# Kernel optimization log

Hardware: AMD Instinct MI355X
Metric: run time of the kernel (lower is better)

Reference implementation:

```python
import jax, jax.numpy as jnp
import numpy as np

B = 2
NCLS = 19    # semantic classes for the logits heads
NLAB = 20    # raw point label values 0..19 (0 = unlabeled)
# (Z, Y, X) grids at strides 2, 4, 8 of sizes=[256,256,32]
GRIDS = {2: (16, 128, 128), 4: (8, 64, 64), 8: (4, 32, 32)}


def _lin_idx(coord, Z, Y, X):
    # coord: (N,4) int rows [b, z, y, x] -> flat cell index over B*Z*Y*X
    b, z, y, x = coord[:, 0], coord[:, 1], coord[:, 2], coord[:, 3]
    return ((b * Z + z) * Y + y) * X + x


def _bev_projection(feat, coord, Y, X):
    # Fused equivalent of torch.unique + scatter_max + spconv dense():
    # scatter_max features directly into the dense (B, Y, X) BEV grid keyed by (b,y,x).
    key = (coord[:, 0] * Y + coord[:, 2]) * X + coord[:, 3]
    C = feat.shape[1]
    dense = jax.ops.segment_max(feat, key, num_segments=B * Y * X)  # empty cells -> -inf
    dense = jnp.where(jnp.isfinite(dense), dense, jnp.zeros((), feat.dtype))
    return dense.reshape(B, Y, X, C).transpose(0, 3, 1, 2)  # (B, C, Y, X)


def _voxel_sem_target(fcoord, pcoord, plabel, Z, Y, X):
    # Majority-vote semantic label per point voxel, gathered at feature voxel coords.
    ncell = B * Z * Y * X
    pair = _lin_idx(pcoord, Z, Y, X) * NLAB + plabel  # (cell, label) key
    counts = jax.ops.segment_sum(
        jnp.ones(pcoord.shape[0], jnp.int32), pair, num_segments=ncell * NLAB
    ).reshape(ncell, NLAB)
    maj = jnp.argmax(counts, axis=1).astype(jnp.int32)   # most frequent label per cell
    occ = counts.sum(axis=1) > 0                          # cell contains any point
    fk = _lin_idx(fcoord, Z, Y, X)
    return jnp.where(occ[fk], maj[fk], 0).astype(jnp.int32)  # unmatched -> 0


def _head(x, w1, g, b, w2, b2):
    # Linear(no bias) -> BatchNorm1d(train stats) -> LeakyReLU(0.1) -> Linear
    h = x @ w1
    mu = h.mean(axis=0)
    var = h.var(axis=0)
    h = (h - mu) * jax.lax.rsqrt(var + 1e-5) * g + b
    h = jnp.where(h >= 0, h, 0.1 * h)
    return h @ w2 + b2


def _rand_coords(key, n, Z, Y, X):
    kb, kz, ky, kx = jax.random.split(key, 4)
    return jnp.stack([
        jax.random.randint(kb, (n,), 0, B, dtype=jnp.int32),
        jax.random.randint(kz, (n,), 0, Z, dtype=jnp.int32),
        jax.random.randint(ky, (n,), 0, Y, dtype=jnp.int32),
        jax.random.randint(kx, (n,), 0, X, dtype=jnp.int32),
    ], axis=1)


def setup_inputs() -> dict:
    key = jax.random.key(0)
    ks = jax.random.split(key, 32)
    M1, M2, M3, NP = 200000, 100000, 50000, 500000
    inp = {
        'proj1_vw': jax.random.normal(ks[0], (M1, 64), jnp.float32),
        'proj2_vw': jax.random.normal(ks[1], (M2, 128), jnp.float32),
        'proj3_vw': jax.random.normal(ks[2], (M3, 256), jnp.float32),
        'vw1_coord': _rand_coords(ks[3], M1, *GRIDS[2]),
        'vw2_coord': _rand_coords(ks[4], M2, *GRIDS[4]),
        'vw3_coord': _rand_coords(ks[5], M3, *GRIDS[8]),
        'idx02': _rand_coords(ks[6], NP, *GRIDS[2]),
        'idx04': _rand_coords(ks[7], NP, *GRIDS[4]),
        'idx08': _rand_coords(ks[8], NP, *GRIDS[8]),
        'pw_label': jax.random.randint(ks[9], (NP,), 0, NLAB, dtype=jnp.int32),
    }
    # learned head parameters (out2 / out4 / out8)
    def head_params(k, cin):
        k1, k2 = jax.random.split(k)
        return (jax.random.normal(k1, (cin, 64), jnp.float32) * 0.02,
                jnp.ones((64,), jnp.float32), jnp.zeros((64,), jnp.float32),
                jax.random.normal(k2, (64, NCLS), jnp.float32) * 0.02,
                jnp.zeros((NCLS,), jnp.float32))
    for tag, k, cin in (('h2', ks[10], 64), ('h4', ks[11], 128), ('h8', ks[12], 256)):
        w1, g, b, w2, b2 = head_params(k, cin)
        inp[f'{tag}_w1'], inp[f'{tag}_g'], inp[f'{tag}_b'] = w1, g, b
        inp[f'{tag}_w2'], inp[f'{tag}_b2'] = w2, b2
    return inp


def reference(proj1_vw, proj2_vw, proj3_vw, vw1_coord, vw2_coord, vw3_coord,
              idx02, idx04, idx08, pw_label,
              h2_w1, h2_g, h2_b, h2_w2, h2_b2,
              h4_w1, h4_g, h4_b, h4_w2, h4_b2,
              h8_w1, h8_g, h8_b, h8_w2, h8_b2):
    (Z2, Y2, X2), (Z4, Y4, X4), (Z8, Y8, X8) = GRIDS[2], GRIDS[4], GRIDS[8]
    bev1 = _bev_projection(proj1_vw, vw1_coord, Y2, X2)   # (B, 64, 128, 128)
    bev2 = _bev_projection(proj2_vw, vw2_coord, Y4, X4)   # (B, 128, 64, 64)
    bev3 = _bev_projection(proj3_vw, vw3_coord, Y8, X8)   # (B, 256, 32, 32)
    lbl2 = _voxel_sem_target(vw1_coord, idx02, pw_label, Z2, Y2, X2)
    lbl4 = _voxel_sem_target(vw2_coord, idx04, pw_label, Z4, Y4, X4)
    lbl8 = _voxel_sem_target(vw3_coord, idx08, pw_label, Z8, Y8, X8)
    log2 = _head(proj1_vw, h2_w1, h2_g, h2_b, h2_w2, h2_b2)
    log4 = _head(proj2_vw, h4_w1, h4_g, h4_b, h4_w2, h4_b2)
    log8 = _head(proj3_vw, h8_w1, h8_g, h8_b, h8_w2, h8_b2)
    return (bev1, bev2, bev3, log2, log4, log8, lbl2, lbl4, lbl8)
```

## Files before the change

### kernel.cpp

```cpp
#include <hip/hip_runtime.h>
#include <hip/hip_bf16.h>

typedef unsigned int u32;
typedef unsigned short u16;
typedef __attribute__((ext_vector_type(8))) short short8;
typedef __attribute__((ext_vector_type(4))) float f32x4;

#define NLAB 20

#define M_1 200000
#define C_1 64
#define Z_1 16
#define Y_1 128
#define X_1 128

#define M_2 100000
#define C_2 128
#define Z_2 8
#define Y_2 64
#define X_2 64

#define M_3 50000
#define C_3 256
#define Z_3 4
#define Y_3 32
#define X_3 32

#define O_BEV1 0
#define O_BEV2 2097152
#define O_BEV3 3145728
#define O_LOG1 3670016
#define O_LOG2 7470016
#define O_LOG3 9370016
#define O_LBL1 10320016
#define O_LBL2 10520016
#define O_LBL3 10620016

#define WB_CNT 0
#define WB_CUR 43008
#define WB_PIDX 86016
#define NCELLS 43008
#define SB1 0
#define SB2 32768
#define SB3 40960

#define WBEV_F  4194304
#define WBEV2_F 6291456
#define WBEV3_F 7340032

#define WC1_W 8388608
#define WC2_W 11010048
#define WC3_W 11337728
#define W_COUNT_BYTES 11960320ull
#define WH1 0
#define WH2 12800000
#define WH3 19200000
#define WPART 12000000
#define WP1 0
#define WP2 200064
#define WP3 300160
#define WSTATS 12350208

#define GB1 1563
#define GB2 782
#define GB3 391
#define HB1 782
#define HB2 391
#define HB3 196

static __device__ __forceinline__ u16 f2bf(float f) {
  u32 u = __float_as_uint(f);
  u32 r = u + 0x7fffu + ((u >> 16) & 1u);
  return (u16)(r >> 16);
}

__global__ __launch_bounds__(256) void k_cellcount(
    const int* __restrict__ co1, const int* __restrict__ co2, const int* __restrict__ co3,
    int* __restrict__ cnt)
{
  int blk = blockIdx.x;
  const int* co; int Y, X, M, base, m;
  if (blk < HB1)            { co = co1; Y = Y_1; X = X_1; M = M_1; base = SB1; m = blk * 256 + threadIdx.x; }
  else if (blk < HB1 + HB2) { co = co2; Y = Y_2; X = X_2; M = M_2; base = SB2; m = (blk - HB1) * 256 + threadIdx.x; }
  else                      { co = co3; Y = Y_3; X = X_3; M = M_3; base = SB3; m = (blk - HB1 - HB2) * 256 + threadIdx.x; }
  if (m >= M) return;
  int4 c = *(const int4*)(co + m * 4);
  atomicAdd(cnt + base + (c.x * Y + c.z) * X + c.w, 1);
}

__global__ __launch_bounds__(1024) void k_scan(const int* __restrict__ cnt, int* __restrict__ cur) {
  int t = threadIdx.x;
  int local[42];
  int s = 0;
#pragma unroll
  for (int j = 0; j < 42; j++) { local[j] = cnt[t * 42 + j]; s += local[j]; }
  __shared__ int red[1024];
  red[t] = s;
  __syncthreads();
  for (int off = 1; off < 1024; off <<= 1) {
    int v = (t >= off) ? red[t - off] : 0;
    __syncthreads();
    red[t] += v;
    __syncthreads();
  }
  int base = red[t] - s;
#pragma unroll
  for (int j = 0; j < 42; j++) { cur[t * 42 + j] = base; base += local[j]; }
}

__global__ __launch_bounds__(256) void k_scatter(
    const int* __restrict__ co1, const int* __restrict__ co2, const int* __restrict__ co3,
    int* __restrict__ cur, int* __restrict__ pidx)
{
  int blk = blockIdx.x;
  const int* co; int Y, X, M, base, m;
  if (blk < HB1)            { co = co1; Y = Y_1; X = X_1; M = M_1; base = SB1; m = blk * 256 + threadIdx.x; }
  else if (blk < HB1 + HB2) { co = co2; Y = Y_2; X = X_2; M = M_2; base = SB2; m = (blk - HB1) * 256 + threadIdx.x; }
  else                      { co = co3; Y = Y_3; X = X_3; M = M_3; base = SB3; m = (blk - HB1 - HB2) * 256 + threadIdx.x; }
  if (m >= M) return;
  int4 c = *(const int4*)(co + m * 4);
  int slot = atomicAdd(cur + base + (c.x * Y + c.z) * X + c.w, 1);
  pidx[slot] = m;
}

#define GBATCH 8
__global__ __launch_bounds__(256) void k_gc(
    const float* __restrict__ f1, const float* __restrict__ f2, const float* __restrict__ f3,
    const int* __restrict__ cnt, const int* __restrict__ cur,
    const int* __restrict__ pidx, float* __restrict__ ws,
    const int* __restrict__ i2, const int* __restrict__ i4, const int* __restrict__ i8,
    const int* __restrict__ lab, u32* __restrict__ hist)
{
  int blk = blockIdx.x;
  if (blk < 14336) {
    int wid = blk * 4 + (threadIdx.x >> 6);
    int lane = threadIdx.x & 63;
    const float* f; int cidx; size_t wbase; int C;
    if (wid < 32768) {
      f = f1; C = 64; cidx = SB1 + wid; wbase = WBEV_F + (size_t)wid * 64;
    } else if (wid < 49152) {
      int u = wid - 32768; int cell = u >> 1, ch = (u & 1) * 64;
      f = f2 + ch; C = 128; cidx = SB2 + cell; wbase = WBEV2_F + (size_t)cell * 128 + ch;
    } else {
      int u = wid - 49152; int cell = u >> 2, ch = (u & 3) * 64;
      f = f3 + ch; C = 256; cidx = SB3 + cell; wbase = WBEV3_F + (size_t)cell * 256 + ch;
    }
    int n = cnt[cidx], end = cur[cidx];
    float acc = __uint_as_float(0xff800000u);
    for (int i = end - n; i < end; i += GBATCH) {
      int p[GBATCH];
#pragma unroll
      for (int j = 0; j < GBATCH; j++) {
        int idx = i + j;
        p[j] = pidx[idx < end ? idx : end - 1];
      }
      float v[GBATCH];
#pragma unroll
      for (int j = 0; j < GBATCH; j++) v[j] = f[(size_t)p[j] * C + lane];
#pragma unroll
      for (int j = 0; j < GBATCH; j++) acc = fmaxf(acc, v[j]);
    }
    ws[wbase + lane] = (n > 0) ? acc : 0.f;
  } else {
    int cb = blk - 14336;
    const int* pc; int Z, Y, X; u32* base; int i;
    if (cb < 1954)      { pc = i2; Z = Z_1; Y = Y_1; X = X_1; base = hist + WC1_W; i = cb * 256 + threadIdx.x; }
    else if (cb < 3908) { pc = i4; Z = Z_2; Y = Y_2; X = X_2; base = hist + WC2_W; i = (cb - 1954) * 256 + threadIdx.x; }
    else                { pc = i8; Z = Z_3; Y = Y_3; X = X_3; base = hist + WC3_W; i = (cb - 3908) * 256 + threadIdx.x; }
    if (i >= 500000) return;
    int4 c = *(const int4*)(pc + i * 4);
    int l = lab[i];
    int lin = ((c.x * Z + c.y) * Y + c.z) * X + c.w;
    atomicAdd(base + lin * 5 + (l >> 2), 1u << ((l & 3) * 8));
  }
}

__global__ __launch_bounds__(256) void k_tl(
    const float* __restrict__ ws, const u32* __restrict__ hist,
    const int* __restrict__ fc1, const int* __restrict__ fc2, const int* __restrict__ fc3,
    float* __restrict__ out)
{
  int blk = blockIdx.x;
  int tid = threadIdx.x;
  if (blk < HB1 + HB2 + HB3) {
    const int* fc; int Z, Y, X, M; const u32* base; long lbase; int m;
    if (blk < HB1)            { fc = fc1; Z = Z_1; Y = Y_1; X = X_1; M = M_1; base = hist + WC1_W; lbase = O_LBL1; m = blk * 256 + tid; }
    else if (blk < HB1 + HB2) { fc = fc2; Z = Z_2; Y = Y_2; X = X_2; M = M_2; base = hist + WC2_W; lbase = O_LBL2; m = (blk - HB1) * 256 + tid; }
    else                      { fc = fc3; Z = Z_3; Y = Y_3; X = X_3; M = M_3; base = hist + WC3_W; lbase = O_LBL3; m = (blk - HB1 - HB2) * 256 + tid; }
    if (m >= M) return;
    int4 c = *(const int4*)(fc + m * 4);
    int lin = ((c.x * Z + c.y) * Y + c.z) * X + c.w;
    const u32* cp = base + lin * 5;
    u32 w0 = cp[0], w1 = cp[1], w2 = cp[2], w3 = cp[3], w4 = cp[4];
    int best = (int)(w0 & 0xffu); int bi = 0;
#pragma unroll
    for (int n = 1; n < NLAB; n++) {
      u32 w = (n < 4) ? w0 : (n < 8) ? w1 : (n < 12) ? w2 : (n < 16) ? w3 : w4;
      int cc = (int)((w >> ((n & 3) * 8)) & 0xffu);
      if (cc > best) { best = cc; bi = n; }
    }
    out[lbase + m] = (float)bi;
    return;
  }
  __shared__ float tileU[4160];
  int bid = blk - (HB1 + HB2 + HB3);
  if (bid < 512) {
    int b = bid >> 8, y = (bid >> 1) & 127, x0 = (bid & 1) * 64;
    const float* src = ws + WBEV_F + (size_t)((b * 128 + y) * 128 + x0) * 64;
#pragma unroll
    for (int pass = 0; pass < 16; pass++) {
      int idx = pass * 256 + tid;
      int x = idx >> 6, c = idx & 63;
      tileU[x * 65 + c] = src[(size_t)x * 64 + c];
    }
    __syncthreads();
    size_t ob = O_BEV1 + ((size_t)(b * 64) * 128 + y) * 128 + x0;
#pragma unroll
    for (int pass = 0; pass < 16; pass++) {
      int idx = pass * 256 + tid;
      int c = idx >> 6, x = idx & 63;
      out[ob + (size_t)c * 16384 + x] = tileU[x * 65 + c];
    }
  } else if (bid < 768) {
    int t = bid - 512;
    int b = t >> 7, y = (t >> 1) & 63, x0 = (t & 1) * 32;
    const float* src = ws + WBEV2_F + (size_t)((b * 64 + y) * 64 + x0) * 128;
#pragma unroll
    for (int pass = 0; pass < 16; pass++) {
      int idx = pass * 256 + tid;
      int x = idx >> 7, c = idx & 127;
      tileU[x * 129 + c] = src[(size_t)x * 128 + c];
    }
    __syncthreads();
    size_t ob = O_BEV2 + ((size_t)(b * 128) * 64 + y) * 64 + x0;
#pragma unroll
    for (int pass = 0; pass < 16; pass++) {
      int idx = pass * 256 + tid;
      int c = idx >> 5, x = idx & 31;
      out[ob + (size_t)c * 4096 + x] = tileU[x * 129 + c];
    }
  } else {
    int t = bid - 768;
    int b = t >> 6, y = (t >> 1) & 31, ch0 = (t & 1) * 128;
    const float* src = ws + WBEV3_F + (size_t)((b * 32 + y) * 32) * 256 + ch0;
#pragma unroll
    for (int pass = 0; pass < 16; pass++) {
      int idx = pass * 256 + tid;
      int x = idx >> 7, c = idx & 127;
      tileU[x * 129 + c] = src[(size_t)x * 256 + c];
    }
    __syncthreads();
    size_t ob = O_BEV3 + ((size_t)(b * 256 + ch0) * 32 + y) * 32;
#pragma unroll
    for (int pass = 0; pass < 16; pass++) {
      int idx = pass * 256 + tid;
      int c = idx >> 5, x = idx & 31;
      out[ob + (size_t)c * 1024 + x] = tileU[x * 129 + c];
    }
  }
}

__global__ __launch_bounds__(256) void k_gemm(
    const float* __restrict__ x1, const float* __restrict__ x2, const float* __restrict__ x3,
    const float* __restrict__ w1a, const float* __restrict__ w1b, const float* __restrict__ w1c,
    u16* __restrict__ hbuf, float* __restrict__ part)
{
  int blk = blockIdx.x;
  const float* x; const float* w1; u16* h; float* pp; int Cin, M, bl, NB;
  if (blk < GB1)            { x = x1; w1 = w1a; h = hbuf + WH1; pp = part + WP1; Cin = C_1; M = M_1; bl = blk;             NB = GB1; }
  else if (blk < GB1 + GB2) { x = x2; w1 = w1b; h = hbuf + WH2; pp = part + WP2; Cin = C_2; M = M_2; bl = blk - GB1;       NB = GB2; }
  else                      { x = x3; w1 = w1c; h = hbuf + WH3; pp = part + WP3; Cin = C_3; M = M_3; bl = blk - GB1 - GB2; NB = GB3; }
  int tid = threadIdx.x;
  int lane = tid & 63, wv = tid >> 6;
  int m16 = lane & 15, quad = lane >> 4;

  __shared__ u16 As[128 * 72];
  __shared__ u16 Bs[64 * 72];
  __shared__ float redS[4][64];
  __shared__ float redQ[4][64];

  f32x4 acc[2][4];
#pragma unroll
  for (int mt = 0; mt < 2; mt++)
#pragma unroll
    for (int nt = 0; nt < 4; nt++) acc[mt][nt] = (f32x4){0.f, 0.f, 0.f, 0.f};

  int nchunk = Cin >> 6;
  for (int c = 0; c < nchunk; c++) {
    if (c) __syncthreads();
#pragma unroll
    for (int pass = 0; pass < 8; pass++) {
      int fidx = pass * 256 + tid;
      int row = fidx >> 4, kp = (fidx & 15) * 4;
      int grow = bl * 128 + row;
      float4 v = make_float4(0.f, 0.f, 0.f, 0.f);
      if (grow < M) v = *(const float4*)(x + (size_t)grow * Cin + c * 64 + kp);
      ushort4 o = { f2bf(v.x), f2bf(v.y), f2bf(v.z), f2bf(v.w) };
      *(ushort4*)(As + row * 72 + kp) = o;
    }
    {
      int n = tid & 63, kg = tid >> 6;
#pragma unroll
      for (int p = 0; p < 4; p++) {
        int k0 = kg * 4 + p * 16;
        const float* wp = w1 + (size_t)(c * 64 + k0) * 64 + n;
        ushort4 o = { f2bf(wp[0]), f2bf(wp[64]), f2bf(wp[128]), f2bf(wp[192]) };
        *(ushort4*)(Bs + n * 72 + k0) = o;
      }
    }
    __syncthreads();
#pragma unroll
    for (int ks = 0; ks < 2; ks++) {
      short8 a0 = *(const short8*)(As + (wv * 32 + m16) * 72 + ks * 32 + quad * 8);
      short8 a1 = *(const short8*)(As + (wv * 32 + 16 + m16) * 72 + ks * 32 + quad * 8);
      short8 b[4];
#pragma unroll
      for (int nt = 0; nt < 4; nt++)
        b[nt] = *(const short8*)(Bs + (nt * 16 + m16) * 72 + ks * 32 + quad * 8);
#pragma unroll
      for (int nt = 0; nt < 4; nt++) {
        acc[0][nt] = __builtin_amdgcn_mfma_f32_16x16x32_bf16(a0, b[nt], acc[0][nt], 0, 0, 0);
        acc[1][nt] = __builtin_amdgcn_mfma_f32_16x16x32_bf16(a1, b[nt], acc[1][nt], 0, 0, 0);
      }
    }
  }

  float s[4] = {0.f, 0.f, 0.f, 0.f}, q[4] = {0.f, 0.f, 0.f, 0.f};
#pragma unroll
  for (int mt = 0; mt < 2; mt++) {
#pragma unroll
    for (int nt = 0; nt < 4; nt++) {
#pragma unroll
      for (int r = 0; r < 4; r++) {
        float v = acc[mt][nt][r];
        int grow = bl * 128 + wv * 32 + mt * 16 + quad * 4 + r;
        if (grow < M) h[(size_t)grow * 64 + nt * 16 + m16] = f2bf(v);
        s[nt] += v;
        q[nt] = fmaf(v, v, q[nt]);
      }
    }
  }
#pragma unroll
  for (int nt = 0; nt < 4; nt++) {
    s[nt] += __shfl_xor(s[nt], 16); s[nt] += __shfl_xor(s[nt], 32);
    q[nt] += __shfl_xor(q[nt], 16); q[nt] += __shfl_xor(q[nt], 32);
  }
  if (lane < 16) {
#pragma unroll
    for (int nt = 0; nt < 4; nt++) {
      redS[wv][nt * 16 + lane] = s[nt];
      redQ[wv][nt * 16 + lane] = q[nt];
    }
  }
  __syncthreads();
  if (tid < 64) {
    pp[tid * NB + bl] = redS[0][tid] + redS[1][tid] + redS[2][tid] + redS[3][tid];
  } else if (tid < 128) {
    int n2 = tid - 64;
    pp[(64 + n2) * NB + bl] = redQ[0][n2] + redQ[1][n2] + redQ[2][n2] + redQ[3][n2];
  }
}

__global__ __launch_bounds__(256) void k_stats(const float* __restrict__ part, float* __restrict__ stats,
    const float* __restrict__ g1, const float* __restrict__ b1,
    const float* __restrict__ g4, const float* __restrict__ b4,
    const float* __restrict__ g8, const float* __restrict__ b8)
{
  int blk = blockIdx.x;
  int sc = blk >> 6, col = blk & 63;
  int nb; const float* p; float invM; const float* g; const float* bb;
  if (sc == 0)      { nb = GB1; p = part + WP1; invM = 1.f / M_1; g = g1; bb = b1; }
  else if (sc == 1) { nb = GB2; p = part + WP2; invM = 1.f / M_2; g = g4; bb = b4; }
  else              { nb = GB3; p = part + WP3; invM = 1.f / M_3; g = g8; bb = b8; }
  int t = threadIdx.x;
  const float* ps = p + (size_t)col * nb;
  const float* pq = p + (size_t)(64 + col) * nb;
  float s = 0.f, q = 0.f;
  for (int i = t; i < nb; i += 256) { s += ps[i]; q += pq[i]; }
  __shared__ float r1[256], r2[256];
  r1[t] = s; r2[t] = q;
  __syncthreads();
  for (int off = 128; off > 0; off >>= 1) {
    if (t < off) { r1[t] += r1[t + off]; r2[t] += r2[t + off]; }
    __syncthreads();
  }
  if (t == 0) {
    float mu  = r1[0] * invM;
    float var = r2[0] * invM - mu * mu;
    float scale = rsqrtf(var + 1e-5f) * g[col];
    stats[sc * 128 + col]      = scale;
    stats[sc * 128 + 64 + col] = fmaf(-mu, scale, bb[col]);
  }
}

__global__ __launch_bounds__(256) void k_head(
    const u16* __restrict__ hbuf, const float* __restrict__ stats,
    const float* __restrict__ w21, const float* __restrict__ c21,
    const float* __restrict__ w24, const float* __restrict__ c24,
    const float* __restrict__ w28, const float* __restrict__ c28,
    float* __restrict__ out)
{
  int blk = blockIdx.x;
  const u16* h; const float* st; const float* w2; const float* b2;
  int M; long obase; int bl;
  if (blk < HB1)            { h = hbuf + WH1; st = stats;       w2 = w21; b2 = c21; M = M_1; obase = O_LOG1; bl = blk; }
  else if (blk < HB1 + HB2) { h = hbuf + WH2; st = stats + 128; w2 = w24; b2 = c24; M = M_2; obase = O_LOG2; bl = blk - HB1; }
  else                      { h = hbuf + WH3; st = stats + 256; w2 = w28; b2 = c28; M = M_3; obase = O_LOG3; bl = blk - HB1 - HB2; }
  int tid = threadIdx.x;
  int rowbase = bl * 256;
  int avail = M - rowbase; if (avail > 256) avail = 256;

  __shared__ __align__(16) float os[256 * 19];

  float acc[19];
#pragma unroll
  for (int n = 0; n < 19; n++) acc[n] = 0.f;

  if (tid < avail) {
    const uint4* hr = (const uint4*)(h + (size_t)(rowbase + tid) * 64);
    uint4 d[8];
#pragma unroll
    for (int q = 0; q < 8; q++) d[q] = hr[q];
#pragma unroll
    for (int q = 0; q < 8; q++) {
#pragma unroll
      for (int half = 0; half < 2; half++) {
        u32 dx = half ? d[q].z : d[q].x;
        u32 dy = half ? d[q].w : d[q].y;
        int j = q * 8 + half * 4;
        float f0 = __uint_as_float(dx << 16);
        float f1 = __uint_as_float(dx & 0xffff0000u);
        float f2 = __uint_as_float(dy << 16);
        float f3 = __uint_as_float(dy & 0xffff0000u);
        float a0 = fmaf(f0, st[j],     st[64 + j]);     a0 = a0 >= 0.f ? a0 : 0.1f * a0;
        float a1 = fmaf(f1, st[j + 1], st[64 + j + 1]); a1 = a1 >= 0.f ? a1 : 0.1f * a1;
        float a2 = fmaf(f2, st[j + 2], st[64 + j + 2]); a2 = a2 >= 0.f ? a2 : 0.1f * a2;
        float a3 = fmaf(f3, st[j + 3], st[64 + j + 3]); a3 = a3 >= 0.f ? a3 : 0.1f * a3;
#pragma unroll
        for (int n = 0; n < 19; n++) {
          acc[n] = fmaf(a0, w2[j * 19 + n], acc[n]);
          acc[n] = fmaf(a1, w2[(j + 1) * 19 + n], acc[n]);
          acc[n] = fmaf(a2, w2[(j + 2) * 19 + n], acc[n]);
          acc[n] = fmaf(a3, w2[(j + 3) * 19 + n], acc[n]);
        }
      }
    }
#pragma unroll
    for (int n = 0; n < 19; n++) os[tid * 19 + n] = acc[n] + b2[n];
  }
  __syncthreads();
  int tot = avail * 19;
  float* op = out + obase + (size_t)rowbase * 19;
  for (int i = tid; i < tot; i += 256) op[i] = os[i];
}

extern "C" void kernel_launch(void* const* d_in, const int* in_sizes, int n_in,
                              void* d_out, int out_size, void* d_ws, size_t ws_size,
                              hipStream_t stream) {
  (void)in_sizes; (void)n_in; (void)out_size; (void)ws_size;
  const float* p1 = (const float*)d_in[0];
  const float* p2 = (const float*)d_in[1];
  const float* p3 = (const float*)d_in[2];
  const int* vc1  = (const int*)d_in[3];
  const int* vc2  = (const int*)d_in[4];
  const int* vc3  = (const int*)d_in[5];
  const int* i2   = (const int*)d_in[6];
  const int* i4   = (const int*)d_in[7];
  const int* i8   = (const int*)d_in[8];
  const int* lab  = (const int*)d_in[9];
  const float* h2w1 = (const float*)d_in[10]; const float* h2g = (const float*)d_in[11];
  const float* h2b  = (const float*)d_in[12]; const float* h2w2 = (const float*)d_in[13];
  const float* h2b2 = (const float*)d_in[14];
  const float* h4w1 = (const float*)d_in[15]; const float* h4g = (const float*)d_in[16];
  const float* h4b  = (const float*)d_in[17]; const float* h4w2 = (const float*)d_in[18];
  const float* h4b2 = (const float*)d_in[19];
  const float* h8w1 = (const float*)d_in[20]; const float* h8g = (const float*)d_in[21];
  const float* h8b  = (const float*)d_in[22]; const float* h8w2 = (const float*)d_in[23];
  const float* h8b2 = (const float*)d_in[24];

  float* out = (float*)d_out;
  int* wsi = (int*)d_ws;
  u32* wsu = (u32*)d_ws;
  float* wsf = (float*)d_ws;
  u16* wsh = (u16*)d_ws;

  hipMemsetAsync(wsi + WB_CNT, 0, NCELLS * sizeof(int), stream);
  hipMemsetAsync(wsu + WC1_W, 0, W_COUNT_BYTES, stream);

  k_cellcount<<<HB1 + HB2 + HB3, 256, 0, stream>>>(vc1, vc2, vc3, wsi + WB_CNT);
  k_scan<<<1, 1024, 0, stream>>>(wsi + WB_CNT, wsi + WB_CUR);
  k_scatter<<<HB1 + HB2 + HB3, 256, 0, stream>>>(vc1, vc2, vc3, wsi + WB_CUR, wsi + WB_PIDX);

  k_gc<<<14336 + 5862, 256, 0, stream>>>(p1, p2, p3,
      wsi + WB_CNT, wsi + WB_CUR, wsi + WB_PIDX, wsf,
      i2, i4, i8, lab, wsu);

  k_tl<<<HB1 + HB2 + HB3 + 896, 256, 0, stream>>>(wsf, wsu, vc1, vc2, vc3, out);

  k_gemm<<<GB1 + GB2 + GB3, 256, 0, stream>>>(p1, p2, p3, h2w1, h4w1, h8w1, wsh, wsf + WPART);
  k_stats<<<192, 256, 0, stream>>>(wsf + WPART, wsf + WSTATS, h2g, h2b, h4g, h4b, h8g, h8b);
  k_head<<<HB1 + HB2 + HB3, 256, 0, stream>>>((const u16*)d_ws, wsf + WSTATS,
      h2w2, h2b2, h4w2, h4b2, h8w2, h8b2, out);
}
```

Baseline: 460.0 us.

## Move label histogram into cell-count kernel and gather four BEV tasks per wave

The point-label histogram atomics move out of the gather kernel and into the cell-count kernel, so they overlap with the cell counting instead of with the BEV max-gather. The BEV gather kernel now gives each wave four (cell, channel-slice) tasks and interleaves their loads, which raises memory-level parallelism and cuts the grid from 14336 blocks to 3584. In exchange, each wave loops to the largest count among its four tasks, adding redundant clamped loads, and register pressure goes up.

```diff
diff --git a/kernel.cpp b/kernel.cpp
--- a/kernel.cpp
+++ b/kernel.cpp
@@ -74,18 +74,33 @@
   return (u16)(r >> 16);
 }
 
-__global__ __launch_bounds__(256) void k_cellcount(
+__global__ __launch_bounds__(256) void k_cc(
     const int* __restrict__ co1, const int* __restrict__ co2, const int* __restrict__ co3,
-    int* __restrict__ cnt)
+    int* __restrict__ cnt,
+    const int* __restrict__ i2, const int* __restrict__ i4, const int* __restrict__ i8,
+    const int* __restrict__ lab, u32* __restrict__ hist)
 {
   int blk = blockIdx.x;
-  const int* co; int Y, X, M, base, m;
-  if (blk < HB1)            { co = co1; Y = Y_1; X = X_1; M = M_1; base = SB1; m = blk * 256 + threadIdx.x; }
-  else if (blk < HB1 + HB2) { co = co2; Y = Y_2; X = X_2; M = M_2; base = SB2; m = (blk - HB1) * 256 + threadIdx.x; }
-  else                      { co = co3; Y = Y_3; X = X_3; M = M_3; base = SB3; m = (blk - HB1 - HB2) * 256 + threadIdx.x; }
-  if (m >= M) return;
-  int4 c = *(const int4*)(co + m * 4);
-  atomicAdd(cnt + base + (c.x * Y + c.z) * X + c.w, 1);
+  if (blk < HB1 + HB2 + HB3) {
+    const int* co; int Y, X, M, base, m;
+    if (blk < HB1)            { co = co1; Y = Y_1; X = X_1; M = M_1; base = SB1; m = blk * 256 + threadIdx.x; }
+    else if (blk < HB1 + HB2) { co = co2; Y = Y_2; X = X_2; M = M_2; base = SB2; m = (blk - HB1) * 256 + threadIdx.x; }
+    else                      { co = co3; Y = Y_3; X = X_3; M = M_3; base = SB3; m = (blk - HB1 - HB2) * 256 + threadIdx.x; }
+    if (m >= M) return;
+    int4 c = *(const int4*)(co + m * 4);
+    atomicAdd(cnt + base + (c.x * Y + c.z) * X + c.w, 1);
+  } else {
+    int cb = blk - (HB1 + HB2 + HB3);
+    const int* pc; int Z, Y, X; u32* base; int i;
+    if (cb < 1954)      { pc = i2; Z = Z_1; Y = Y_1; X = X_1; base = hist + WC1_W; i = cb * 256 + threadIdx.x; }
+    else if (cb < 3908) { pc = i4; Z = Z_2; Y = Y_2; X = X_2; base = hist + WC2_W; i = (cb - 1954) * 256 + threadIdx.x; }
+    else                { pc = i8; Z = Z_3; Y = Y_3; X = X_3; base = hist + WC3_W; i = (cb - 3908) * 256 + threadIdx.x; }
+    if (i >= 500000) return;
+    int4 c = *(const int4*)(pc + i * 4);
+    int l = lab[i];
+    int lin = ((c.x * Z + c.y) * Y + c.z) * X + c.w;
+    atomicAdd(base + lin * 5 + (l >> 2), 1u << ((l & 3) * 8));
+  }
 }
 
 __global__ __launch_bounds__(1024) void k_scan(const int* __restrict__ cnt, int* __restrict__ cur) {
@@ -124,55 +139,63 @@
 }
 
 #define GBATCH 8
-__global__ __launch_bounds__(256) void k_gc(
+__global__ __launch_bounds__(256) void k_bevgather(
     const float* __restrict__ f1, const float* __restrict__ f2, const float* __restrict__ f3,
     const int* __restrict__ cnt, const int* __restrict__ cur,
-    const int* __restrict__ pidx, float* __restrict__ ws,
-    const int* __restrict__ i2, const int* __restrict__ i4, const int* __restrict__ i8,
-    const int* __restrict__ lab, u32* __restrict__ hist)
-{
-  int blk = blockIdx.x;
-  if (blk < 14336) {
-    int wid = blk * 4 + (threadIdx.x >> 6);
-    int lane = threadIdx.x & 63;
-    const float* f; int cidx; size_t wbase; int C;
-    if (wid < 32768) {
-      f = f1; C = 64; cidx = SB1 + wid; wbase = WBEV_F + (size_t)wid * 64;
-    } else if (wid < 49152) {
-      int u = wid - 32768; int cell = u >> 1, ch = (u & 1) * 64;
-      f = f2 + ch; C = 128; cidx = SB2 + cell; wbase = WBEV2_F + (size_t)cell * 128 + ch;
+    const int* __restrict__ pidx, float* __restrict__ ws)
+{
+  int w = blockIdx.x * 4 + (threadIdx.x >> 6);
+  int lane = threadIdx.x & 63;
+  int t0 = w * 4;
+  int C = (t0 < 32768) ? 64 : (t0 < 49152) ? 128 : 256;
+  const float* fp[4]; int n[4], end_[4]; u32 wb[4];
+#pragma unroll
+  for (int k = 0; k < 4; k++) {
+    int t = t0 + k; const float* f; int cidx; u32 wbv;
+    if (t < 32768) {
+      f = f1; cidx = SB1 + t; wbv = WBEV_F + (u32)t * 64;
+    } else if (t < 49152) {
+      int u = t - 32768; int cell = u >> 1, ch = (u & 1) * 64;
+      f = f2 + ch; cidx = SB2 + cell; wbv = WBEV2_F + (u32)cell * 128 + ch;
     } else {
-      int u = wid - 49152; int cell = u >> 2, ch = (u & 3) * 64;
-      f = f3 + ch; C = 256; cidx = SB3 + cell; wbase = WBEV3_F + (size_t)cell * 256 + ch;
-    }
-    int n = cnt[cidx], end = cur[cidx];
-    float acc = __uint_as_float(0xff800000u);
-    for (int i = end - n; i < end; i += GBATCH) {
-      int p[GBATCH];
+      int u = t - 49152; int cell = u >> 2, ch = (u & 3) * 64;
+      f = f3 + ch; cidx = SB3 + cell; wbv = WBEV3_F + (u32)cell * 256 + ch;
+    }
+    fp[k] = f; n[k] = cnt[cidx]; end_[k] = cur[cidx]; wb[k] = wbv;
+  }
+  int maxn = max(max(n[0], n[1]), max(n[2], n[3]));
+  float acc[4];
+#pragma unroll
+  for (int k = 0; k < 4; k++) acc[k] = __uint_as_float(0xff800000u);
+  for (int base = 0; base < maxn; base += GBATCH) {
+    int p[4][GBATCH];
+#pragma unroll
+    for (int k = 0; k < 4; k++) {
+      int s = end_[k] - n[k] + base;
+      int hi = end_[k] - 1;
 #pragma unroll
       for (int j = 0; j < GBATCH; j++) {
-        int idx = i + j;
-        p[j] = pidx[idx < end ? idx : end - 1];
+        int idx = s + j;
+        idx = idx < hi ? idx : hi;
+        idx = idx > 0 ? idx : 0;
+        p[k][j] = pidx[idx];
       }
-      float v[GBATCH];
-#pragma unroll
-      for (int j = 0; j < GBATCH; j++) v[j] = f[(size_t)p[j] * C + lane];
-#pragma unroll
-      for (int j = 0; j < GBATCH; j++) acc = fmaxf(acc, v[j]);
-    }
-    ws[wbase + lane] = (n > 0) ? acc : 0.f;
-  } else {
-    int cb = blk - 14336;
-    const int* pc; int Z, Y, X; u32* base; int i;
-    if (cb < 1954)      { pc = i2; Z = Z_1; Y = Y_1; X = X_1; base = hist + WC1_W; i = cb * 256 + threadIdx.x; }
-    else if (cb < 3908) { pc = i4; Z = Z_2; Y = Y_2; X = X_2; base = hist + WC2_W; i = (cb - 1954) * 256 + threadIdx.x; }
-    else                { pc = i8; Z = Z_3; Y = Y_3; X = X_3; base = hist + WC3_W; i = (cb - 3908) * 256 + threadIdx.x; }
-    if (i >= 500000) return;
-    int4 c = *(const int4*)(pc + i * 4);
-    int l = lab[i];
-    int lin = ((c.x * Z + c.y) * Y + c.z) * X + c.w;
-    atomicAdd(base + lin * 5 + (l >> 2), 1u << ((l & 3) * 8));
-  }
+    }
+    float v[4][GBATCH];
+#pragma unroll
+    for (int k = 0; k < 4; k++)
+#pragma unroll
+      for (int j = 0; j < GBATCH; j++)
+        v[k][j] = fp[k][(size_t)p[k][j] * C + lane];
+#pragma unroll
+    for (int k = 0; k < 4; k++)
+#pragma unroll
+      for (int j = 0; j < GBATCH; j++)
+        acc[k] = fmaxf(acc[k], v[k][j]);
+  }
+#pragma unroll
+  for (int k = 0; k < 4; k++)
+    ws[wb[k] + lane] = (n[k] > 0) ? acc[k] : 0.f;
 }
 
 __global__ __launch_bounds__(256) void k_tl(
@@ -487,13 +510,13 @@
   hipMemsetAsync(wsi + WB_CNT, 0, NCELLS * sizeof(int), stream);
   hipMemsetAsync(wsu + WC1_W, 0, W_COUNT_BYTES, stream);
 
-  k_cellcount<<<HB1 + HB2 + HB3, 256, 0, stream>>>(vc1, vc2, vc3, wsi + WB_CNT);
+  k_cc<<<HB1 + HB2 + HB3 + 5862, 256, 0, stream>>>(vc1, vc2, vc3, wsi + WB_CNT,
+      i2, i4, i8, lab, wsu);
   k_scan<<<1, 1024, 0, stream>>>(wsi + WB_CNT, wsi + WB_CUR);
   k_scatter<<<HB1 + HB2 + HB3, 256, 0, stream>>>(vc1, vc2, vc3, wsi + WB_CUR, wsi + WB_PIDX);
 
-  k_gc<<<14336 + 5862, 256, 0, stream>>>(p1, p2, p3,
-      wsi + WB_CNT, wsi + WB_CUR, wsi + WB_PIDX, wsf,
-      i2, i4, i8, lab, wsu);
+  k_bevgather<<<3584, 256, 0, stream>>>(p1, p2, p3,
+      wsi + WB_CNT, wsi + WB_CUR, wsi + WB_PIDX, wsf);
 
   k_tl<<<HB1 + HB2 + HB3 + 896, 256, 0, stream>>>(wsf, wsu, vc1, vc2, vc3, out);
 
```

Measured after the change: 464.2 us. No clear change (+0.9%).
